# Optimization experiments

Hardware: AMD Instinct MI355X
Metric: run time of the kernel (lower is better)

## Reference

```python
import jax, jax.numpy as jnp
import numpy as np

N = 128          # cube side (voxels)
LPIX = 3.0       # Mpc per voxel (hardcoded in dsq_loss.forward)
KBINS = 100      # radial k bins (hardcoded)
LOSS_WEIGHT = 1.0


def _binning(n, lpix, kbins):
    # Static radial k-bin assignment computed once with numpy.
    kf = 2.0 * np.pi * np.fft.fftfreq(n, d=lpix)
    kx, ky, kz = np.meshgrid(kf, kf, kf, indexing='ij')
    kmag = np.sqrt(kx * kx + ky * ky + kz * kz).ravel()  # [n^3]
    pos = kmag > 0
    edges = np.linspace(kmag[pos].min(), kmag.max(), kbins + 1)
    ids = np.clip(np.digitize(kmag, edges) - 1, 0, kbins - 1)
    ids = np.where(pos, ids, kbins)  # route k=0 (DC) mode to a dropped bin
    counts = np.bincount(ids[pos], minlength=kbins).astype(np.float32)
    kcent = 0.5 * (edges[:-1] + edges[1:])
    return ids.astype(np.int32), counts, kcent.astype(np.float32)

_IDS, _COUNTS, _KCENT = _binning(N, LPIX, KBINS)


def _dsq(x):
    # x: [B, 1, N, N, N] -> dimensionless power spectrum Delta^2(k): [B, KBINS]
    b = x.shape[0]
    fk = jnp.fft.fftn(x, axes=(-3, -2, -1))
    # P(k) estimator: |delta_k|^2 * Lpix^3 / N^3  (Lpix^6/V with V=(N*Lpix)^3)
    pk = (fk.real ** 2 + fk.imag ** 2) * (LPIX ** 3 / float(N ** 3))
    pk = pk.reshape(b, -1).T  # [N^3, B]
    sums = jax.ops.segment_sum(pk, jnp.asarray(_IDS), num_segments=KBINS + 1)[:KBINS]
    cnt = jnp.asarray(_COUNTS)[:, None]
    pmean = jnp.where(cnt > 0, sums / jnp.maximum(cnt, 1.0), jnp.nan)  # [KBINS, B]
    kc = jnp.asarray(_KCENT)[:, None]
    dsq = pmean * kc ** 3 / (2.0 * jnp.pi ** 2)
    return dsq.T  # [B, KBINS]


def setup_inputs() -> dict:
    key = jax.random.key(0)
    k1, k2 = jax.random.split(key)
    # positive brightness-temperature-like fields so log10(Delta^2) is finite
    pred = jax.random.uniform(k1, (8, 1, N, N, N), dtype=jnp.float32) + 0.1
    target = jax.random.uniform(k2, (8, 1, N, N, N), dtype=jnp.float32) + 0.1
    return {"pred": pred, "target": target}


def reference(pred, target):
    dsq_hr = _dsq(target)
    dsq_sr = _dsq(pred)
    loss = jnp.nanmean(jnp.abs(jnp.log10(dsq_hr) - jnp.log10(dsq_sr)))
    return LOSS_WEIGHT * loss
```

## Files before the change

kernel.cpp:

```cpp
#include <hip/hip_runtime.h>
#include <math.h>

#ifndef M_PI
#define M_PI 3.14159265358979323846
#endif

#define NSIDE 128
#define NVOX  2097152
#define KBINS 100
#define NFIELDS 16
#define NORMF (27.0f / 2097152.0f)
#define FSTRIDE ((size_t)65 * 16384)

#define WS_SUMS_OFF   0
#define WS_CNT_OFF    6464
#define WS_OCT_OFF    8192
#define WS_TRANS_OFF  282880

__device__ __forceinline__ double bin_edge(int i, double start, double step, double stop) {
    if (i == 100) return stop;
    return __dadd_rn(__dmul_rn((double)i, step), start);
}

__device__ __forceinline__ void bin_params(double* start, double* step, double* stop) {
    const double inv   = 1.0 / 384.0;
    const double twopi = 2.0 * M_PI;
    double k1 = __dmul_rn(twopi, __dmul_rn(1.0, inv));
    *start = sqrt(__dadd_rn(__dadd_rn(0.0, 0.0), __dmul_rn(k1, k1)));
    double k64 = __dmul_rn(twopi, __dmul_rn(-64.0, inv));
    double s64 = __dmul_rn(k64, k64);
    *stop = sqrt(__dadd_rn(__dadd_rn(s64, s64), s64));
    *step = (*stop - *start) / 100.0;
}

__device__ int compute_bin(int ix, int iy, int iz) {
    const double inv   = 1.0 / 384.0;
    const double twopi = 2.0 * M_PI;
    double fx = (double)(ix < 64 ? ix : ix - 128);
    double fy = (double)(iy < 64 ? iy : iy - 128);
    double fz = (double)(iz < 64 ? iz : iz - 128);
    double kx = __dmul_rn(twopi, __dmul_rn(fx, inv));
    double ky = __dmul_rn(twopi, __dmul_rn(fy, inv));
    double kz = __dmul_rn(twopi, __dmul_rn(fz, inv));
    double sq = __dadd_rn(__dadd_rn(__dmul_rn(kx, kx), __dmul_rn(ky, ky)), __dmul_rn(kz, kz));
    double kmag = sqrt(sq);
    if (!(kmag > 0.0)) return 100;
    double start, step, stop;
    bin_params(&start, &step, &stop);
    double t = (kmag - start) / step;
    int c = (int)floor(t);
    if (c < -1) c = -1;
    if (c > 100) c = 100;
    while (c < 100 && kmag >= bin_edge(c + 1, start, step, stop)) ++c;
    while (c >= 0 && kmag < bin_edge(c, start, step, stop)) --c;
    if (c < 0) c = 0;
    if (c > 99) c = 99;
    return c;
}


__device__ __forceinline__ int br3(int v) { return ((v & 1) << 2) | (v & 2) | ((v >> 2) & 1); }
__device__ __forceinline__ int br4(int v) {
    return ((v & 1) << 3) | ((v & 2) << 1) | ((v & 4) >> 1) | ((v & 8) >> 3);
}

__device__ __forceinline__ float2 f2add(float2 a, float2 b) { return make_float2(a.x + b.x, a.y + b.y); }
__device__ __forceinline__ float2 f2sub(float2 a, float2 b) { return make_float2(a.x - b.x, a.y - b.y); }
__device__ __forceinline__ float2 cmul(float2 a, float2 w) {
    return make_float2(a.x * w.x - a.y * w.y, a.x * w.y + a.y * w.x);
}
__device__ __forceinline__ float2 twid(float r) {
    return make_float2(__builtin_amdgcn_cosf(r), __builtin_amdgcn_sinf(r));
}

__device__ __forceinline__ void fft128_r16(float2 r[16], int m) {
    const float fm = (float)m;
#pragma unroll
    for (int j = 0; j < 8; ++j) {
        float2 W = twid(-(fm + 8.0f * (float)j) * (1.0f / 128.0f));
        float2 a = r[j], b = r[j + 8];
        r[j]     = f2add(a, b);
        r[j + 8] = cmul(f2sub(a, b), W);
    }
#pragma unroll
    for (int j = 0; j < 4; ++j) {
        float2 W = twid(-(fm + 8.0f * (float)j) * (1.0f / 64.0f));
#pragma unroll
        for (int half = 0; half < 16; half += 8) {
            float2 a = r[half + j], b = r[half + j + 4];
            r[half + j]     = f2add(a, b);
            r[half + j + 4] = cmul(f2sub(a, b), W);
        }
    }
#pragma unroll
    for (int j = 0; j < 2; ++j) {
        float2 W = twid(-(fm + 8.0f * (float)j) * (1.0f / 32.0f));
#pragma unroll
        for (int q = 0; q < 16; q += 4) {
            float2 a = r[q + j], b = r[q + j + 2];
            r[q + j]     = f2add(a, b);
            r[q + j + 2] = cmul(f2sub(a, b), W);
        }
    }
    {
        float2 W = twid(-fm * (1.0f / 16.0f));
#pragma unroll
        for (int q = 0; q < 16; q += 2) {
            float2 a = r[q], b = r[q + 1];
            r[q]     = f2add(a, b);
            r[q + 1] = cmul(f2sub(a, b), W);
        }
    }
#pragma unroll
    for (int h = 4; h >= 2; h >>= 1) {
        bool hi = (m & h) != 0;
        float2 W = twid(-(float)(m & (h - 1)) / (float)(2 * h));
#pragma unroll
        for (int j = 0; j < 16; ++j) {
            float2 x = r[j];
            float2 v = make_float2(__shfl_xor(x.x, h, 64), __shfl_xor(x.y, h, 64));
            float2 s = f2add(x, v);
            float2 d = cmul(f2sub(v, x), W);
            r[j] = hi ? d : s;
        }
    }
    {
        bool hi = (m & 1) != 0;
#pragma unroll
        for (int j = 0; j < 16; ++j) {
            float2 x = r[j];
            float2 v = make_float2(__shfl_xor(x.x, 1, 64), __shfl_xor(x.y, 1, 64));
            r[j] = hi ? f2sub(v, x) : f2add(x, v);
        }
    }
}

__global__ __launch_bounds__(256) void k_zero(float* sums, int* counts) {
    int t = blockIdx.x * 256 + threadIdx.x;
    if (t < NFIELDS * 101) sums[t] = 0.0f;
    if (t < 101) counts[t] = 0;
}

__global__ __launch_bounds__(256) void k_oct(unsigned char* __restrict__ oct,
                                             int* __restrict__ counts) {
    __shared__ int lcnt[4][104];
    int tid = threadIdx.x;
#pragma unroll
    for (int j = tid; j < 4 * 104; j += 256) ((int*)lcnt)[j] = 0;
    __syncthreads();
    int idx = blockIdx.x * 256 + tid;
    if (idx < 65 * 65 * 65) {
        int c = idx % 65;
        int r = idx / 65;
        int b = r % 65;
        int a = r / 65;
        int id = compute_bin(a, b, c);
        oct[c * 4225 + a * 65 + b] = (unsigned char)id;
        if (id < 100) {
            int w = ((a == 0 || a == 64) ? 1 : 2) *
                    ((b == 0 || b == 64) ? 1 : 2) *
                    ((c == 0 || c == 64) ? 1 : 2);
            atomicAdd(&lcnt[tid & 3][id], w);
        }
    }
    __syncthreads();
    if (tid < 101) {
        int tot = lcnt[0][tid] + lcnt[1][tid] + lcnt[2][tid] + lcnt[3][tid];
        if (tot) atomicAdd(&counts[tid], tot);
    }
}

__global__ __launch_bounds__(256, 6) void k_fft_z(const float* __restrict__ pred,
                                                  const float* __restrict__ target,
                                                  float2* __restrict__ A) {
    int t = threadIdx.x;
    int m = t & 7, row = t >> 3;
    int x  = blockIdx.x >> 2;
    int y0 = (blockIdx.x & 3) << 5;
    int f = blockIdx.y;
    const float* in = (f < 8) ? (pred + (size_t)f * NVOX)
                              : (target + (size_t)(f - 8) * NVOX);
    const float* src = in + (size_t)x * 16384 + (size_t)(y0 + row) * 128;
    float2 r[16];
#pragma unroll
    for (int j = 0; j < 16; ++j) r[j] = make_float2(src[m + 8 * j], 0.0f);
    fft128_r16(r, m);
    float2* dst = A + (size_t)f * FSTRIDE + (size_t)x * 128 + (y0 + row);
    int b3 = br3(m);
    if (b3 < 4) {
#pragma unroll
        for (int j = 0; j < 16; ++j) {
            int kz = 16 * b3 + br4(j);
            dst[(size_t)kz * 16384] = r[j];
        }
    } else if (b3 == 4) {
        dst[(size_t)64 * 16384] = r[0];
    }
}

__global__ __launch_bounds__(256, 6) void k_fft_y(float2* __restrict__ A) {
    int t = threadIdx.x;
    int m = t & 7, g = t >> 3;
    int kz = blockIdx.x >> 2;
    int xg = blockIdx.x & 3;
    int f = blockIdx.y;
    float2* base = A + (size_t)f * FSTRIDE + (size_t)kz * 16384
                     + (size_t)(xg * 32 + g) * 128;
    float2 r[16];
#pragma unroll
    for (int j = 0; j < 16; ++j) r[j] = base[m + 8 * j];
    fft128_r16(r, m);
#pragma unroll
    for (int j = 0; j < 16; ++j) base[m + 8 * j] = r[j];
}

__global__ __launch_bounds__(256, 6) void k_fft_x_bin(const float2* __restrict__ A,
                                                      const unsigned char* __restrict__ oct,
                                                      float* __restrict__ sums) {
    __shared__ float lbins[8][104];
    __shared__ unsigned char ltab[4225];
    int t = threadIdx.x;
    int m = t & 7, g = t >> 3;
    int kz = blockIdx.x >> 2;
    int s0 = (blockIdx.x & 3) << 5;
    int f = blockIdx.y;
    for (int j = t; j < 8 * 104; j += 256) ((float*)lbins)[j] = 0.0f;
    for (int j = t; j < 4225; j += 256) ltab[j] = oct[kz * 4225 + j];
    const float2* base = A + (size_t)f * FSTRIDE + (size_t)kz * 16384 + (s0 + g);
    float2 r[16];
#pragma unroll
    for (int j = 0; j < 16; ++j) r[j] = base[(size_t)(m + 8 * j) * 128];
    fft128_r16(r, m);
    __syncthreads();
    int p = s0 + g;
    int ky = (br3(p & 7) << 4) | br4(p >> 3);
    int mky = (ky <= 64) ? ky : 128 - ky;
    int b3x = br3(m) << 4;
#pragma unroll
    for (int j = 0; j < 16; ++j) {
        int kx = b3x | br4(j);
        int mkx = (kx <= 64) ? kx : 128 - kx;
        float pk = r[j].x * r[j].x + r[j].y * r[j].y;
        atomicAdd(&lbins[t & 7][ltab[mkx * 65 + mky]], pk);
    }
    __syncthreads();
    if (t < 101) {
        float wz = (kz == 0 || kz == 64) ? 1.0f : 2.0f;
        float v = lbins[0][t] + lbins[1][t] + lbins[2][t] + lbins[3][t] +
                  lbins[4][t] + lbins[5][t] + lbins[6][t] + lbins[7][t];
        if (v != 0.0f) atomicAdd(&sums[f * 101 + t], v * (NORMF) * wz);
    }
}

__global__ __launch_bounds__(128) void k_finalize(const float* __restrict__ sums,
                                                  const int* __restrict__ counts,
                                                  float* __restrict__ out) {
    __shared__ double ssum[128];
    __shared__ int scnt[128];
    int k = threadIdx.x;
    double local = 0.0;
    int nloc = 0;
    if (k < KBINS) {
        int c = counts[k];
        if (c > 0) {
            double start, step, stop;
            bin_params(&start, &step, &stop);
            double e0 = bin_edge(k, start, step, stop);
            double e1 = bin_edge(k + 1, start, step, stop);
            float kc  = (float)(0.5 * (e0 + e1));
            float kc3 = kc * kc * kc;
            const float two_pi2 = (float)(2.0 * M_PI * M_PI);
            float cf = (float)c;
            for (int b = 0; b < 8; ++b) {
                float pm_p = sums[b * 101 + k] / cf;
                float pm_t = sums[(8 + b) * 101 + k] / cf;
                float dsq_p = pm_p * kc3 / two_pi2;
                float dsq_t = pm_t * kc3 / two_pi2;
                float d = fabsf(log10f(dsq_t) - log10f(dsq_p));
                local += (double)d;
            }
            nloc = 8;
        }
    }
    ssum[k] = local;
    scnt[k] = nloc;
    __syncthreads();
    for (int off = 64; off > 0; off >>= 1) {
        if (k < off) { ssum[k] += ssum[k + off]; scnt[k] += scnt[k + off]; }
        __syncthreads();
    }
    if (k == 0) out[0] = (float)(ssum[0] / (double)scnt[0]);
}

extern "C" void kernel_launch(void* const* d_in, const int* in_sizes, int n_in,
                              void* d_out, int out_size, void* d_ws, size_t ws_size,
                              hipStream_t stream) {
    (void)in_sizes; (void)n_in; (void)out_size; (void)ws_size;
    const float* pred   = (const float*)d_in[0];
    const float* target = (const float*)d_in[1];
    float* out = (float*)d_out;
    char* ws = (char*)d_ws;

    float* sums        = (float*)(ws + WS_SUMS_OFF);
    int* counts        = (int*)(ws + WS_CNT_OFF);
    unsigned char* oct = (unsigned char*)(ws + WS_OCT_OFF);
    float2* A          = (float2*)(ws + WS_TRANS_OFF);

    k_zero<<<7, 256, 0, stream>>>(sums, counts);
    k_oct<<<(65 * 65 * 65 + 255) / 256, 256, 0, stream>>>(oct, counts);

    k_fft_z<<<dim3(512, NFIELDS), 256, 0, stream>>>(pred, target, A);
    k_fft_y<<<dim3(65 * 4, NFIELDS), 256, 0, stream>>>(A);
    k_fft_x_bin<<<dim3(65 * 4, NFIELDS), 256, 0, stream>>>(A, oct, sums);

    k_finalize<<<1, 128, 0, stream>>>(sums, counts, out);
}
```

Baseline: 342.3 us.

## Fuse y and x FFT passes into one per-plane kernel using LDS transpose

The separate y-FFT and x-FFT+binning kernels become one kernel where a 1024-thread block handles a whole 128x128 kz-plane. It does the y-direction FFT on rows, transposes through a padded 128x130 shared-memory tile, then runs the x-direction FFT and bins the power. This removes one full global read/write round trip of the intermediate spectrum and one launch. In exchange it uses about 133KB of LDS per block and 1024-thread blocks, which sharply reduces occupancy, and it drops the occupancy hint on k_fft_z.

```diff
diff --git a/kernel.cpp b/kernel.cpp
--- a/kernel.cpp
+++ b/kernel.cpp
@@ -170,9 +170,9 @@
     }
 }
 
-__global__ __launch_bounds__(256, 6) void k_fft_z(const float* __restrict__ pred,
-                                                  const float* __restrict__ target,
-                                                  float2* __restrict__ A) {
+__global__ __launch_bounds__(256) void k_fft_z(const float* __restrict__ pred,
+                                               const float* __restrict__ target,
+                                               float2* __restrict__ A) {
     int t = threadIdx.x;
     int m = t & 7, row = t >> 3;
     int x  = blockIdx.x >> 2;
@@ -198,42 +198,30 @@
     }
 }
 
-__global__ __launch_bounds__(256, 6) void k_fft_y(float2* __restrict__ A) {
-    int t = threadIdx.x;
-    int m = t & 7, g = t >> 3;
-    int kz = blockIdx.x >> 2;
-    int xg = blockIdx.x & 3;
-    int f = blockIdx.y;
-    float2* base = A + (size_t)f * FSTRIDE + (size_t)kz * 16384
-                     + (size_t)(xg * 32 + g) * 128;
-    float2 r[16];
-#pragma unroll
-    for (int j = 0; j < 16; ++j) r[j] = base[m + 8 * j];
-    fft128_r16(r, m);
-#pragma unroll
-    for (int j = 0; j < 16; ++j) base[m + 8 * j] = r[j];
-}
-
-__global__ __launch_bounds__(256, 6) void k_fft_x_bin(const float2* __restrict__ A,
-                                                      const unsigned char* __restrict__ oct,
-                                                      float* __restrict__ sums) {
+__global__ __launch_bounds__(1024) void k_plane2(const float2* __restrict__ A,
+                                                 const unsigned char* __restrict__ oct,
+                                                 float* __restrict__ sums) {
+    __shared__ float2 P[128][130];
     __shared__ float lbins[8][104];
     __shared__ unsigned char ltab[4225];
     int t = threadIdx.x;
+    int kz = blockIdx.x, f = blockIdx.y;
+    const float2* plane = A + (size_t)f * FSTRIDE + (size_t)kz * 16384;
+    for (int j = t; j < 8 * 104; j += 1024) ((float*)lbins)[j] = 0.0f;
+    for (int j = t; j < 4225; j += 1024) ltab[j] = oct[kz * 4225 + j];
     int m = t & 7, g = t >> 3;
-    int kz = blockIdx.x >> 2;
-    int s0 = (blockIdx.x & 3) << 5;
-    int f = blockIdx.y;
-    for (int j = t; j < 8 * 104; j += 256) ((float*)lbins)[j] = 0.0f;
-    for (int j = t; j < 4225; j += 256) ltab[j] = oct[kz * 4225 + j];
-    const float2* base = A + (size_t)f * FSTRIDE + (size_t)kz * 16384 + (s0 + g);
     float2 r[16];
-#pragma unroll
-    for (int j = 0; j < 16; ++j) r[j] = base[(size_t)(m + 8 * j) * 128];
+    const float2* rowp = plane + (size_t)g * 128;
+#pragma unroll
+    for (int j = 0; j < 16; ++j) r[j] = rowp[m + 8 * j];
     fft128_r16(r, m);
-    __syncthreads();
-    int p = s0 + g;
-    int ky = (br3(p & 7) << 4) | br4(p >> 3);
+#pragma unroll
+    for (int j = 0; j < 16; ++j) P[g][m + 8 * j] = r[j];
+    __syncthreads();
+#pragma unroll
+    for (int j = 0; j < 16; ++j) r[j] = P[m + 8 * j][g];
+    fft128_r16(r, m);
+    int ky = (br3(g & 7) << 4) | br4(g >> 3);
     int mky = (ky <= 64) ? ky : 128 - ky;
     int b3x = br3(m) << 4;
 #pragma unroll
@@ -310,8 +298,7 @@
     k_oct<<<(65 * 65 * 65 + 255) / 256, 256, 0, stream>>>(oct, counts);
 
     k_fft_z<<<dim3(512, NFIELDS), 256, 0, stream>>>(pred, target, A);
-    k_fft_y<<<dim3(65 * 4, NFIELDS), 256, 0, stream>>>(A);
-    k_fft_x_bin<<<dim3(65 * 4, NFIELDS), 256, 0, stream>>>(A, oct, sums);
+    k_plane2<<<dim3(65, NFIELDS), 1024, 0, stream>>>(A, oct, sums);
 
     k_finalize<<<1, 128, 0, stream>>>(sums, counts, out);
 }
```

Measured after the change: 358.4 us. 4.7% more time.
